# Kernel optimization log

Hardware: AMD Instinct MI355X
Metric: run time of the kernel (lower is better)

## Reference

```python
import jax, jax.numpy as jnp
import numpy as np

B, T, N, F, D, E = 8, 256, 118, 3, 128, 372
G = B * T  # number of graphs after flattening batch*time


def _gcn(x, src, dst, W, b):
    # x: [G, N, Fin] -> PyG GCNConv: X' = D^-1/2 (A+I) D^-1/2 (X W) + b
    h = x @ W  # [G, N, Fout]
    deg = jnp.ones((N,), h.dtype).at[dst].add(1.0)  # in-degree + self loop
    inv = deg ** -0.5
    norm = inv[src] * inv[dst]  # [E]
    agg = h * (1.0 / deg)[None, :, None]  # self-loop term: inv[i]*inv[i] = 1/deg
    agg = agg.at[:, dst].add(h[:, src] * norm[None, :, None])
    return agg + b


def _lstm_layer(x, Wih, Whh, bih, bhh):
    # x: [B, T, I]; PyTorch gate order i, f, g, o
    Bb, H = x.shape[0], Whh.shape[1]
    h0 = jnp.zeros((Bb, H), x.dtype)
    c0 = jnp.zeros((Bb, H), x.dtype)

    def step(carry, xt):
        h, c = carry
        gates = xt @ Wih.T + h @ Whh.T + bih + bhh
        i, f, g, o = jnp.split(gates, 4, axis=-1)
        c = jax.nn.sigmoid(f) * c + jax.nn.sigmoid(i) * jnp.tanh(g)
        h = jax.nn.sigmoid(o) * jnp.tanh(c)
        return (h, c), h

    _, ys = jax.lax.scan(step, (h0, c0), jnp.swapaxes(x, 0, 1))
    return jnp.swapaxes(ys, 0, 1)


def setup_inputs() -> dict:
    key = jax.random.key(0)
    ks = jax.random.split(key, 24)
    s = 0.05

    def rn(i, shape):
        return jax.random.normal(ks[i], shape, jnp.float32) * s

    return {
        "snapshot_sequence": jax.random.normal(ks[0], (B, T, N, F), jnp.float32),
        "edge_index": jax.random.randint(ks[1], (2, E), 0, N, dtype=jnp.int64),
        "scale": jnp.ones((F,), jnp.float32),
        "shift": jnp.zeros((F,), jnp.float32),
        "W1": rn(2, (F, D)), "b1": jnp.zeros((D,), jnp.float32),
        "W2": rn(3, (D, D)), "b2": jnp.zeros((D,), jnp.float32),
        "W3": rn(4, (D, D)), "b3": jnp.zeros((D,), jnp.float32),
        "Wih0": rn(5, (4 * D, D)), "Whh0": rn(6, (4 * D, D)),
        "bih0": jnp.zeros((4 * D,), jnp.float32), "bhh0": jnp.zeros((4 * D,), jnp.float32),
        "Wih1": rn(7, (4 * D, D)), "Whh1": rn(8, (4 * D, D)),
        "bih1": jnp.zeros((4 * D,), jnp.float32), "bhh1": jnp.zeros((4 * D,), jnp.float32),
        "hW1": rn(9, (D, 128)), "hb1": jnp.zeros((128,), jnp.float32),
        "hW2": rn(10, (128, 64)), "hb2": jnp.zeros((64,), jnp.float32),
        "hW3": rn(11, (64, 2)), "hb3": jnp.zeros((2,), jnp.float32),
    }


def reference(snapshot_sequence, edge_index, scale, shift,
              W1, b1, W2, b2, W3, b3,
              Wih0, Whh0, bih0, bhh0, Wih1, Whh1, bih1, bhh1,
              hW1, hb1, hW2, hb2, hW3, hb3):
    src, dst = edge_index[0], edge_index[1]
    x = snapshot_sequence * scale + shift              # FeatureNormalizer
    x = x.reshape(G, N, F)                             # flatten batch*time graphs
    x = jax.nn.silu(_gcn(x, src, dst, W1, b1))         # GCNConv 1 (dropout = eval identity)
    x = jax.nn.silu(_gcn(x, src, dst, W2, b2))         # GCNConv 2
    x = jax.nn.silu(_gcn(x, src, dst, W3, b3))         # GCNConv 3
    emb = x.mean(axis=1)                               # global_mean_pool -> [G, D]
    emb = emb.reshape(B, T, D)
    h = _lstm_layer(emb, Wih0, Whh0, bih0, bhh0)       # 2-layer LSTM (eval: no dropout)
    h = _lstm_layer(h, Wih1, Whh1, bih1, bhh1)
    final = h[:, -1, :]                                # [B, D]
    y = jax.nn.silu(final @ hW1 + hb1)
    y = jax.nn.silu(y @ hW2 + hb2)
    y = y @ hW3 + hb3
    return jax.nn.softplus(y) + 1e-6                   # [B, 2]
```

## Files before the change

kernel.cpp:

```cpp
#include <hip/hip_runtime.h>
#include <math.h>

#define NN 118
#define EE 372
#define GG 2048
#define DD 128
#define TT 256
#define BB 8
#define FD 512

#define XS 136

typedef short bf16x8 __attribute__((ext_vector_type(8)));
typedef float f32x4  __attribute__((ext_vector_type(4)));
typedef _Float16 f16x2 __attribute__((ext_vector_type(2)));

__device__ __forceinline__ float frcp_(float x) { return __builtin_amdgcn_rcpf(x); }
__device__ __forceinline__ float sig_f(float x) { return frcp_(1.0f + __expf(-x)); }
__device__ __forceinline__ float tanh_f(float x) { return 1.0f - 2.0f * frcp_(__expf(2.0f * x) + 1.0f); }
__device__ __forceinline__ float silu_f(float x) { return x * frcp_(1.0f + __expf(-x)); }
__device__ __forceinline__ float siluf_(float x) { return x / (1.0f + expf(-x)); }

__device__ __forceinline__ float fdot2_(unsigned int a, unsigned int b, float c) {
#if defined(__has_builtin) && __has_builtin(__builtin_amdgcn_fdot2)
    return __builtin_amdgcn_fdot2(__builtin_bit_cast(f16x2, a),
                                  __builtin_bit_cast(f16x2, b), c, false);
#else
    f16x2 x = __builtin_bit_cast(f16x2, a), y = __builtin_bit_cast(f16x2, b);
    return c + (float)x[0] * (float)y[0] + (float)x[1] * (float)y[1];
#endif
}

__device__ __forceinline__ void bar_lds() {
    asm volatile("s_waitcnt lgkmcnt(0)\n\ts_barrier" ::: "memory");
}

__device__ __forceinline__ unsigned short f2bf(float x) {
    unsigned int u = __float_as_uint(x);
    unsigned int r = (u + 0x7fffu + ((u >> 16) & 1u)) >> 16;
    return (unsigned short)r;
}
__device__ __forceinline__ float bf2f(unsigned short b) {
    return __uint_as_float(((unsigned int)b) << 16);
}

__global__ void prep_kernel(const int* __restrict__ ei,
                            const float* __restrict__ bih0, const float* __restrict__ bhh0,
                            const float* __restrict__ bih1, const float* __restrict__ bhh1,
                            float* __restrict__ bias0, float* __restrict__ bias1,
                            unsigned short* __restrict__ AbG) {
    __shared__ int sflag;
    __shared__ int ssrc[EE], sdst[EE];
    __shared__ int scount[NN];
    __shared__ float sinv[NN];
    __shared__ float Adense[NN * NN];
    int tid = threadIdx.x;
    if (tid == 0) sflag = 0;
    __syncthreads();
    for (int i = tid; i < 2 * EE; i += blockDim.x)
        if ((i & 1) && ei[i] != 0) atomicOr(&sflag, 1);
    __syncthreads();
    bool m64 = (sflag == 0);
    for (int e = tid; e < EE; e += blockDim.x) {
        int s, d;
        if (m64) { s = ei[2 * e]; d = ei[2 * EE + 2 * e]; }
        else     { s = ei[e];     d = ei[EE + e]; }
        s = min(max(s, 0), NN - 1); d = min(max(d, 0), NN - 1);
        ssrc[e] = s; sdst[e] = d;
    }
    for (int n = tid; n < NN; n += blockDim.x) scount[n] = 0;
    for (int i = tid; i < NN * NN; i += blockDim.x) Adense[i] = 0.0f;
    __syncthreads();
    for (int e = tid; e < EE; e += blockDim.x) atomicAdd(&scount[sdst[e]], 1);
    __syncthreads();
    for (int n = tid; n < NN; n += blockDim.x) {
        float deg = 1.0f + (float)scount[n];
        sinv[n] = rsqrtf(deg);
        Adense[n * NN + n] = 1.0f / deg;
    }
    __syncthreads();
    for (int e = tid; e < EE; e += blockDim.x)
        atomicAdd(&Adense[sdst[e] * NN + ssrc[e]], sinv[ssrc[e]] * sinv[sdst[e]]);
    __syncthreads();
    for (int i = tid; i < 128 * 128; i += blockDim.x) {
        int r = i >> 7, c = i & 127;
        AbG[i] = (r < NN && c < NN) ? f2bf(Adense[r * NN + c]) : (unsigned short)0;
    }
    for (int j = tid; j < FD; j += blockDim.x) {
        bias0[j] = bih0[j] + bhh0[j];
        bias1[j] = bih1[j] + bhh1[j];
    }
}

__global__ void convw_kernel(const float* __restrict__ W, unsigned short* __restrict__ out) {
    int i = blockIdx.x * 512 + threadIdx.x;
    int n = i >> 7, k = i & 127;
    out[i] = f2bf(W[k * DD + n]);
}

__global__ void convh_kernel(const float* __restrict__ W, unsigned int* __restrict__ out) {
    int i = blockIdx.x * 512 + threadIdx.x;
    int d = i & 127;
    int rest = i >> 7;
    int quarter = rest & 3;
    int qg = rest >> 2;
    int q = qg & 15, g = qg >> 4;
    const float* row = W + (size_t)(g * 128 + d) * 128 + quarter * 32;
    float a = row[2 * q], b = row[2 * q + 1];
    unsigned short lo = __builtin_bit_cast(unsigned short, (_Float16)a);
    unsigned short hi = __builtin_bit_cast(unsigned short, (_Float16)b);
    out[i] = (unsigned int)lo | ((unsigned int)hi << 16);
}

__global__ void transpose_kernel(const float* __restrict__ in, float* __restrict__ out) {
    int idx = blockIdx.x * blockDim.x + threadIdx.x;
    int j = idx >> 7, k = idx & 127;
    out[k * FD + j] = in[idx];
}

__device__ __forceinline__ void load_m(const unsigned short* __restrict__ src,
                                       unsigned short* __restrict__ dst, int tid) {
    const uint4* s4 = (const uint4*)src;
    for (int c = tid; c < 2048; c += 512) {
        int r = c >> 4, k8 = (c & 15) * 8;
        uint4 v = s4[c];
        *(uint4*)(dst + r * XS + k8) = v;
    }
}

__device__ __forceinline__ void mm_xw(const unsigned short* __restrict__ xb,
                                      const unsigned short* __restrict__ wt,
                                      unsigned short* __restrict__ hS, int tid) {
    int lane = tid & 63, w = tid >> 6;
    int lm = lane & 15, lq = lane >> 4;
    int wm = (w & 1) * 64, wn = (w >> 1) * 32;
    f32x4 acc[4][2];
#pragma unroll
    for (int mt = 0; mt < 4; ++mt)
#pragma unroll
        for (int nt = 0; nt < 2; ++nt) acc[mt][nt] = (f32x4){0.f, 0.f, 0.f, 0.f};
#pragma unroll
    for (int kb = 0; kb < 4; ++kb) {
        int ko = kb * 32 + lq * 8;
        bf16x8 b0 = *(const bf16x8*)(wt + (wn + lm) * XS + ko);
        bf16x8 b1 = *(const bf16x8*)(wt + (wn + 16 + lm) * XS + ko);
#pragma unroll
        for (int mt = 0; mt < 4; ++mt) {
            bf16x8 af = *(const bf16x8*)(xb + (wm + mt * 16 + lm) * XS + ko);
            acc[mt][0] = __builtin_amdgcn_mfma_f32_16x16x32_bf16(af, b0, acc[mt][0], 0, 0, 0);
            acc[mt][1] = __builtin_amdgcn_mfma_f32_16x16x32_bf16(af, b1, acc[mt][1], 0, 0, 0);
        }
    }
#pragma unroll
    for (int mt = 0; mt < 4; ++mt)
#pragma unroll
        for (int nt = 0; nt < 2; ++nt) {
            f32x4 a = acc[mt][nt];
            ushort4 pk;
            pk.x = f2bf(a[0]); pk.y = f2bf(a[1]); pk.z = f2bf(a[2]); pk.w = f2bf(a[3]);
            *(ushort4*)(hS + (wn + nt * 16 + lm) * XS + wm + mt * 16 + lq * 4) = pk;
        }
}

__device__ __forceinline__ void mm_agg(const unsigned short* __restrict__ Ab,
                                       const unsigned short* __restrict__ hS,
                                       unsigned short* __restrict__ xb,
                                       float bn0, float bn1, int tid) {
    int lane = tid & 63, w = tid >> 6;
    int lm = lane & 15, lq = lane >> 4;
    int wm = (w & 1) * 64, wn = (w >> 1) * 32;
    f32x4 acc[4][2];
#pragma unroll
    for (int mt = 0; mt < 4; ++mt)
#pragma unroll
        for (int nt = 0; nt < 2; ++nt) acc[mt][nt] = (f32x4){0.f, 0.f, 0.f, 0.f};
#pragma unroll
    for (int kb = 0; kb < 4; ++kb) {
        int ko = kb * 32 + lq * 8;
        bf16x8 b0 = *(const bf16x8*)(hS + (wn + lm) * XS + ko);
        bf16x8 b1 = *(const bf16x8*)(hS + (wn + 16 + lm) * XS + ko);
#pragma unroll
        for (int mt = 0; mt < 4; ++mt) {
            bf16x8 af = *(const bf16x8*)(Ab + (wm + mt * 16 + lm) * XS + ko);
            acc[mt][0] = __builtin_amdgcn_mfma_f32_16x16x32_bf16(af, b0, acc[mt][0], 0, 0, 0);
            acc[mt][1] = __builtin_amdgcn_mfma_f32_16x16x32_bf16(af, b1, acc[mt][1], 0, 0, 0);
        }
    }
#pragma unroll
    for (int mt = 0; mt < 4; ++mt)
#pragma unroll
        for (int nt = 0; nt < 2; ++nt) {
            float bn = nt ? bn1 : bn0;
            int col = wn + nt * 16 + lm;
#pragma unroll
            for (int i = 0; i < 4; ++i) {
                float v = silu_f(acc[mt][nt][i] + bn);
                xb[(wm + mt * 16 + lq * 4 + i) * XS + col] = f2bf(v);
            }
        }
}

__global__ __launch_bounds__(512) void gcn_kernel(
    const float* __restrict__ xg, const float* __restrict__ scale, const float* __restrict__ shift,
    const float* __restrict__ W1, const float* __restrict__ b1,
    const float* __restrict__ b2, const float* __restrict__ b3,
    const unsigned short* __restrict__ AbG,
    const unsigned short* __restrict__ Wt2g, const unsigned short* __restrict__ Wt3g,
    float* __restrict__ emb) {
    extern __shared__ char smem[];
    unsigned short* xb = (unsigned short*)smem;
    unsigned short* hS = (unsigned short*)(smem + 34816);
    unsigned short* Ab = (unsigned short*)(smem + 69632);
    unsigned short* wt = (unsigned short*)(smem + 104448);
    float* xinL  = (float*)(smem + 139264);
    float* meanS = (float*)(smem + 140688);
    int tid = threadIdx.x;
    int lane = tid & 63, w = tid >> 6;
    int g = blockIdx.x;

    for (int i = tid; i < 2176; i += 512) ((uint4*)hS)[i] = (uint4){0, 0, 0, 0};
    for (int i = tid; i < 170; i += 512) ((uint4*)(xb + NN * XS))[i] = (uint4){0, 0, 0, 0};
    float s0 = scale[0], s1 = scale[1], s2 = scale[2];
    float t0 = shift[0], t1 = shift[1], t2 = shift[2];
    const float* xrow = xg + (size_t)g * (NN * 3);
    for (int i = tid; i < NN * 3; i += 512) {
        int f = i % 3;
        float sc = (f == 0) ? s0 : ((f == 1) ? s1 : s2);
        float sf = (f == 0) ? t0 : ((f == 1) ? t1 : t2);
        xinL[i] = xrow[i] * sc + sf;
    }
    load_m(AbG, Ab, tid);
    load_m(Wt2g, wt, tid);
    int lm = lane & 15;
    int wn = (w >> 1) * 32;
    int n0 = wn + lm, n1 = wn + 16 + lm;
    float b1a = b1[n0], b1b = b1[n1];
    float b2a = b2[n0], b2b = b2[n1];
    float b3a = b3[n0], b3b = b3[n1];
    int dd = lane * 2;
    float2 w10 = *(const float2*)(W1 + dd);
    float2 w11 = *(const float2*)(W1 + DD + dd);
    float2 w12 = *(const float2*)(W1 + 2 * DD + dd);
    bar_lds();
    for (int k = 0; k < 15; ++k) {
        int n = w + 8 * k;
        if (n >= NN) break;
        float x0 = xinL[n * 3], x1 = xinL[n * 3 + 1], x2 = xinL[n * 3 + 2];
        hS[dd * XS + n]       = f2bf(x0 * w10.x + x1 * w11.x + x2 * w12.x);
        hS[(dd + 1) * XS + n] = f2bf(x0 * w10.y + x1 * w11.y + x2 * w12.y);
    }
    bar_lds();
    mm_agg(Ab, hS, xb, b1a, b1b, tid);
    bar_lds();
    mm_xw(xb, wt, hS, tid);
    bar_lds();
    load_m(Wt3g, wt, tid);
    mm_agg(Ab, hS, xb, b2a, b2b, tid);
    bar_lds();
    mm_xw(xb, wt, hS, tid);
    bar_lds();
    mm_agg(Ab, hS, xb, b3a, b3b, tid);
    bar_lds();
    {
        int d = tid & 127, part = tid >> 7;
        int a0 = part * 30;
        int a1 = (a0 + 30 < NN) ? (a0 + 30) : NN;
        float s = 0.f;
        for (int n = a0; n < a1; ++n) s += bf2f(xb[n * XS + d]);
        meanS[part * 128 + d] = s;
    }
    bar_lds();
    if (tid < 128) {
        float s = meanS[tid] + meanS[128 + tid] + meanS[256 + tid] + meanS[384 + tid];
        emb[(size_t)g * DD + tid] = s * (1.0f / (float)NN);
    }
}

__global__ __launch_bounds__(512) void proj_kernel(const float* __restrict__ src,
                                                   const float* __restrict__ WT,
                                                   const float* __restrict__ bias,
                                                   float* __restrict__ dst) {
    __shared__ __align__(16) float eL[DD];
    int g = blockIdx.x, tid = threadIdx.x;
    if (tid < DD) eL[tid] = src[(size_t)g * DD + tid];
    __syncthreads();
    float acc = bias[tid];
    const float* wt = WT + tid;
#pragma unroll 8
    for (int k = 0; k < DD; ++k) acc += eL[k] * wt[(size_t)k * FD];
    dst[(size_t)g * FD + tid] = acc;
}

__global__ __launch_bounds__(512, 2) void scan_kernel(
    const float* __restrict__ inp,
    const unsigned int* __restrict__ Wc,
    float* __restrict__ hout, int full) {
    __shared__ __align__(16) unsigned short hL[DD];
    __shared__ __align__(16) float sgP[3 * DD * 4];
    int b = blockIdx.x, j = threadIdx.x;
    int d = j & 127, quarter = j >> 7;
    unsigned int wreg[4][16];
#pragma unroll
    for (int g = 0; g < 4; ++g)
#pragma unroll
        for (int q = 0; q < 16; ++q)
            wreg[g][q] = Wc[(((g * 16 + q) << 2) + quarter) * 128 + d];
#pragma unroll
    for (int g = 0; g < 4; ++g)
#pragma unroll
        for (int q = 0; q < 16; ++q)
            asm volatile("" : "+v"(wreg[g][q]));
    if (j < 64) ((unsigned int*)hL)[j] = 0u;
    float creg = 0.f;
    const float* ib = inp + (size_t)b * TT * FD;
    float* hb_ = hout + (size_t)b * (full ? TT * DD : DD);
    float xg0[4], xg1[4];
    if (quarter == 0) {
#pragma unroll
        for (int g = 0; g < 4; ++g) { xg0[g] = ib[g * DD + d]; xg1[g] = ib[FD + g * DD + d]; }
    }
    bar_lds();
    for (int t = 0; t < TT; ++t) {
        float xg2[4];
        if (quarter == 0) {
            bool more = (t + 2 < TT);
#pragma unroll
            for (int g = 0; g < 4; ++g)
                xg2[g] = more ? ib[(t + 2) * FD + g * DD + d] : 0.f;
        }
        const uint4* h4 = (const uint4*)(hL + quarter * 32);
        float a0 = 0.f, a1 = 0.f, a2 = 0.f, a3 = 0.f;
#pragma unroll
        for (int c = 0; c < 4; ++c) {
            uint4 hv = h4[c];
            a0 = fdot2_(wreg[0][4 * c + 0], hv.x, a0);
            a1 = fdot2_(wreg[1][4 * c + 0], hv.x, a1);
            a2 = fdot2_(wreg[2][4 * c + 0], hv.x, a2);
            a3 = fdot2_(wreg[3][4 * c + 0], hv.x, a3);
            a0 = fdot2_(wreg[0][4 * c + 1], hv.y, a0);
            a1 = fdot2_(wreg[1][4 * c + 1], hv.y, a1);
            a2 = fdot2_(wreg[2][4 * c + 1], hv.y, a2);
            a3 = fdot2_(wreg[3][4 * c + 1], hv.y, a3);
            a0 = fdot2_(wreg[0][4 * c + 2], hv.z, a0);
            a1 = fdot2_(wreg[1][4 * c + 2], hv.z, a1);
            a2 = fdot2_(wreg[2][4 * c + 2], hv.z, a2);
            a3 = fdot2_(wreg[3][4 * c + 2], hv.z, a3);
            a0 = fdot2_(wreg[0][4 * c + 3], hv.w, a0);
            a1 = fdot2_(wreg[1][4 * c + 3], hv.w, a1);
            a2 = fdot2_(wreg[2][4 * c + 3], hv.w, a2);
            a3 = fdot2_(wreg[3][4 * c + 3], hv.w, a3);
        }
        if (quarter != 0)
            *(float4*)(sgP + ((quarter - 1) * DD + d) * 4) = make_float4(a0, a1, a2, a3);
        bar_lds();
        if (quarter == 0) {
            float4 p1 = *(const float4*)(sgP + d * 4);
            float4 p2 = *(const float4*)(sgP + (DD + d) * 4);
            float4 p3 = *(const float4*)(sgP + (2 * DD + d) * 4);
            float iv = sig_f(a0 + p1.x + p2.x + p3.x + xg0[0]);
            float fv = sig_f(a1 + p1.y + p2.y + p3.y + xg0[1]);
            float gv = tanh_f(a2 + p1.z + p2.z + p3.z + xg0[2]);
            float ov = sig_f(a3 + p1.w + p2.w + p3.w + xg0[3]);
            float cn = fv * creg + iv * gv;
            creg = cn;
            float hn = ov * tanh_f(cn);
            ((_Float16*)hL)[d] = (_Float16)hn;
            if (full) hb_[t * DD + d] = hn;
            else if (t == TT - 1) hb_[d] = hn;
#pragma unroll
            for (int g = 0; g < 4; ++g) { xg0[g] = xg1[g]; xg1[g] = xg2[g]; }
        }
        bar_lds();
    }
}

__global__ void head_kernel(const float* __restrict__ hfin,
                            const float* __restrict__ hW1, const float* __restrict__ hb1,
                            const float* __restrict__ hW2, const float* __restrict__ hb2,
                            const float* __restrict__ hW3, const float* __restrict__ hb3,
                            float* __restrict__ out) {
    __shared__ float fh[BB * DD];
    __shared__ float y1[BB * DD];
    __shared__ float y2[BB * 64];
    int tid = threadIdx.x;
    for (int i = tid; i < BB * DD; i += 256) fh[i] = hfin[i];
    __syncthreads();
    for (int i = tid; i < BB * DD; i += 256) {
        int bb = i >> 7, jj = i & 127;
        float acc = hb1[jj];
        for (int k = 0; k < DD; ++k) acc += fh[(bb << 7) + k] * hW1[(k << 7) + jj];
        y1[i] = siluf_(acc);
    }
    __syncthreads();
    for (int i = tid; i < BB * 64; i += 256) {
        int bb = i >> 6, jj = i & 63;
        float acc = hb2[jj];
        for (int k = 0; k < DD; ++k) acc += y1[(bb << 7) + k] * hW2[(k << 6) + jj];
        y2[i] = siluf_(acc);
    }
    __syncthreads();
    if (tid < BB * 2) {
        int bb = tid >> 1, m = tid & 1;
        float acc = hb3[m];
        for (int k = 0; k < 64; ++k) acc += y2[(bb << 6) + k] * hW3[k * 2 + m];
        float sp = fmaxf(acc, 0.f) + log1pf(expf(-fabsf(acc)));
        out[tid] = sp + 1e-6f;
    }
}

extern "C" void kernel_launch(void* const* d_in, const int* in_sizes, int n_in,
                              void* d_out, int out_size, void* d_ws, size_t ws_size,
                              hipStream_t stream) {
    const float* snap  = (const float*)d_in[0];
    const int*   edges = (const int*)d_in[1];
    const float* scale = (const float*)d_in[2];
    const float* shift = (const float*)d_in[3];
    const float* W1 = (const float*)d_in[4];
    const float* b1 = (const float*)d_in[5];
    const float* W2 = (const float*)d_in[6];
    const float* b2 = (const float*)d_in[7];
    const float* W3 = (const float*)d_in[8];
    const float* b3 = (const float*)d_in[9];
    const float* Wih0 = (const float*)d_in[10];
    const float* Whh0 = (const float*)d_in[11];
    const float* bih0 = (const float*)d_in[12];
    const float* bhh0 = (const float*)d_in[13];
    const float* Wih1 = (const float*)d_in[14];
    const float* Whh1 = (const float*)d_in[15];
    const float* bih1 = (const float*)d_in[16];
    const float* bhh1 = (const float*)d_in[17];
    const float* hW1 = (const float*)d_in[18];
    const float* hb1 = (const float*)d_in[19];
    const float* hW2 = (const float*)d_in[20];
    const float* hb2 = (const float*)d_in[21];
    const float* hW3 = (const float*)d_in[22];
    const float* hb3 = (const float*)d_in[23];

    float* ws = (float*)d_ws;
    float* bias0 = ws + 0;
    float* bias1 = ws + 512;
    unsigned short* AbG  = (unsigned short*)(ws + 1024);
    unsigned short* Wt2g = (unsigned short*)(ws + 9216);
    unsigned short* Wt3g = (unsigned short*)(ws + 17408);
    float* WT0 = ws + 25600;
    float* WT1 = ws + 91136;
    unsigned int* Wc0 = (unsigned int*)(ws + 156672);
    unsigned int* Wc1 = (unsigned int*)(ws + 189440);
    float* emb   = ws + 222208;
    float* inp   = ws + 484352;
    float* h0seq = ws + 1532928;
    float* hfin  = ws + 1795072;

    const int smem_gcn = 142736;
    hipFuncSetAttribute((const void*)gcn_kernel,
                        hipFuncAttributeMaxDynamicSharedMemorySize, smem_gcn);

    prep_kernel<<<1, 256, 0, stream>>>(edges, bih0, bhh0, bih1, bhh1,
                                       bias0, bias1, AbG);
    convw_kernel<<<32, 512, 0, stream>>>(W2, Wt2g);
    convw_kernel<<<32, 512, 0, stream>>>(W3, Wt3g);
    convh_kernel<<<64, 512, 0, stream>>>(Whh0, Wc0);
    convh_kernel<<<64, 512, 0, stream>>>(Whh1, Wc1);
    transpose_kernel<<<128, 512, 0, stream>>>(Wih0, WT0);
    transpose_kernel<<<128, 512, 0, stream>>>(Wih1, WT1);
    gcn_kernel<<<GG, 512, smem_gcn, stream>>>(snap, scale, shift, W1, b1, b2, b3,
                                              AbG, Wt2g, Wt3g, emb);
    proj_kernel<<<GG, 512, 0, stream>>>(emb, WT0, bias0, inp);
    scan_kernel<<<BB, 512, 0, stream>>>(inp, Wc0, h0seq, 1);
    proj_kernel<<<GG, 512, 0, stream>>>(h0seq, WT1, bias1, inp);
    scan_kernel<<<BB, 512, 0, stream>>>(inp, Wc1, hfin, 0);
    head_kernel<<<1, 256, 0, stream>>>(hfin, hW1, hb1, hW2, hb2, hW3, hb3, (float*)d_out);
}
```

Measured before the change: 582.3 us.

## Give each thread one full gate row in LSTM scan, combine gates via DPP

The LSTM recurrence kernel now maps each thread to one gate row (d, g) holding the full 128-wide fp16 weight row in registers, instead of splitting the K dimension into quarters that had to be reduced through shared memory. The four gates of a hidden unit sit in adjacent lanes and are exchanged with DPP quad permutes. One unified sigmoid/tanh formula is evaluated per lane, and the h vector is double-buffered so each step needs one barrier instead of two. The weight-packing kernel is changed to the matching layout. This removes the partial-sum LDS round trip and a barrier per timestep, but needs 64 weight registers per thread and drops occupancy to one block per CU.

```diff
diff --git a/kernel.cpp b/kernel.cpp
--- a/kernel.cpp
+++ b/kernel.cpp
@@ -100,16 +100,13 @@
 
 __global__ void convh_kernel(const float* __restrict__ W, unsigned int* __restrict__ out) {
     int i = blockIdx.x * 512 + threadIdx.x;
-    int d = i & 127;
-    int rest = i >> 7;
-    int quarter = rest & 3;
-    int qg = rest >> 2;
-    int q = qg & 15, g = qg >> 4;
-    const float* row = W + (size_t)(g * 128 + d) * 128 + quarter * 32;
-    float a = row[2 * q], b = row[2 * q + 1];
+    int jj = i >> 6, q = i & 63;
+    int d = jj >> 2, g = jj & 3;
+    const float* row = W + (size_t)(g * 128 + d) * 128 + 2 * q;
+    float a = row[0], b = row[1];
     unsigned short lo = __builtin_bit_cast(unsigned short, (_Float16)a);
     unsigned short hi = __builtin_bit_cast(unsigned short, (_Float16)b);
-    out[i] = (unsigned int)lo | ((unsigned int)hi << 16);
+    out[q * 512 + jj] = (unsigned int)lo | ((unsigned int)hi << 16);
 }
 
 __global__ void transpose_kernel(const float* __restrict__ in, float* __restrict__ out) {
@@ -291,85 +288,61 @@
     dst[(size_t)g * FD + tid] = acc;
 }
 
-__global__ __launch_bounds__(512, 2) void scan_kernel(
+__global__ __launch_bounds__(512, 1) void scan_kernel(
     const float* __restrict__ inp,
     const unsigned int* __restrict__ Wc,
     float* __restrict__ hout, int full) {
-    __shared__ __align__(16) unsigned short hL[DD];
-    __shared__ __align__(16) float sgP[3 * DD * 4];
+    __shared__ __align__(16) unsigned short hB[2][DD];
     int b = blockIdx.x, j = threadIdx.x;
-    int d = j & 127, quarter = j >> 7;
-    unsigned int wreg[4][16];
-#pragma unroll
-    for (int g = 0; g < 4; ++g)
-#pragma unroll
-        for (int q = 0; q < 16; ++q)
-            wreg[g][q] = Wc[(((g * 16 + q) << 2) + quarter) * 128 + d];
-#pragma unroll
-    for (int g = 0; g < 4; ++g)
-#pragma unroll
-        for (int q = 0; q < 16; ++q)
-            asm volatile("" : "+v"(wreg[g][q]));
-    if (j < 64) ((unsigned int*)hL)[j] = 0u;
-    float creg = 0.f;
+    int d = j >> 2, g = j & 3;
+    unsigned int wreg[64];
+#pragma unroll
+    for (int q = 0; q < 64; ++q) wreg[q] = Wc[q * 512 + j];
+#pragma unroll
+    for (int q = 0; q < 64; ++q) asm volatile("" : "+v"(wreg[q]));
+    if (j < 128) ((unsigned int*)hB)[j] = 0u;
     const float* ib = inp + (size_t)b * TT * FD;
     float* hb_ = hout + (size_t)b * (full ? TT * DD : DD);
-    float xg0[4], xg1[4];
-    if (quarter == 0) {
-#pragma unroll
-        for (int g = 0; g < 4; ++g) { xg0[g] = ib[g * DD + d]; xg1[g] = ib[FD + g * DD + d]; }
-    }
+    int poff = g * DD + d;
+    float m1  = (g == 2) ? 2.0f : 1.0f;
+    float nm1 = -m1;
+    float c1  = 1.0f - m1;
+    float creg = 0.f;
+    float xg0 = ib[poff], xg1 = ib[FD + poff];
+    int p = 0;
     bar_lds();
     for (int t = 0; t < TT; ++t) {
-        float xg2[4];
-        if (quarter == 0) {
-            bool more = (t + 2 < TT);
-#pragma unroll
-            for (int g = 0; g < 4; ++g)
-                xg2[g] = more ? ib[(t + 2) * FD + g * DD + d] : 0.f;
-        }
-        const uint4* h4 = (const uint4*)(hL + quarter * 32);
+        float xg2 = (t + 2 < TT) ? ib[(size_t)(t + 2) * FD + poff] : 0.f;
+        const uint4* h4 = (const uint4*)(hB[p]);
         float a0 = 0.f, a1 = 0.f, a2 = 0.f, a3 = 0.f;
 #pragma unroll
-        for (int c = 0; c < 4; ++c) {
+        for (int c = 0; c < 16; ++c) {
             uint4 hv = h4[c];
-            a0 = fdot2_(wreg[0][4 * c + 0], hv.x, a0);
-            a1 = fdot2_(wreg[1][4 * c + 0], hv.x, a1);
-            a2 = fdot2_(wreg[2][4 * c + 0], hv.x, a2);
-            a3 = fdot2_(wreg[3][4 * c + 0], hv.x, a3);
-            a0 = fdot2_(wreg[0][4 * c + 1], hv.y, a0);
-            a1 = fdot2_(wreg[1][4 * c + 1], hv.y, a1);
-            a2 = fdot2_(wreg[2][4 * c + 1], hv.y, a2);
-            a3 = fdot2_(wreg[3][4 * c + 1], hv.y, a3);
-            a0 = fdot2_(wreg[0][4 * c + 2], hv.z, a0);
-            a1 = fdot2_(wreg[1][4 * c + 2], hv.z, a1);
-            a2 = fdot2_(wreg[2][4 * c + 2], hv.z, a2);
-            a3 = fdot2_(wreg[3][4 * c + 2], hv.z, a3);
-            a0 = fdot2_(wreg[0][4 * c + 3], hv.w, a0);
-            a1 = fdot2_(wreg[1][4 * c + 3], hv.w, a1);
-            a2 = fdot2_(wreg[2][4 * c + 3], hv.w, a2);
-            a3 = fdot2_(wreg[3][4 * c + 3], hv.w, a3);
-        }
-        if (quarter != 0)
-            *(float4*)(sgP + ((quarter - 1) * DD + d) * 4) = make_float4(a0, a1, a2, a3);
-        bar_lds();
-        if (quarter == 0) {
-            float4 p1 = *(const float4*)(sgP + d * 4);
-            float4 p2 = *(const float4*)(sgP + (DD + d) * 4);
-            float4 p3 = *(const float4*)(sgP + (2 * DD + d) * 4);
-            float iv = sig_f(a0 + p1.x + p2.x + p3.x + xg0[0]);
-            float fv = sig_f(a1 + p1.y + p2.y + p3.y + xg0[1]);
-            float gv = tanh_f(a2 + p1.z + p2.z + p3.z + xg0[2]);
-            float ov = sig_f(a3 + p1.w + p2.w + p3.w + xg0[3]);
-            float cn = fv * creg + iv * gv;
-            creg = cn;
-            float hn = ov * tanh_f(cn);
-            ((_Float16*)hL)[d] = (_Float16)hn;
-            if (full) hb_[t * DD + d] = hn;
-            else if (t == TT - 1) hb_[d] = hn;
-#pragma unroll
-            for (int g = 0; g < 4; ++g) { xg0[g] = xg1[g]; xg1[g] = xg2[g]; }
-        }
+            a0 = fdot2_(wreg[4 * c + 0], hv.x, a0);
+            a1 = fdot2_(wreg[4 * c + 1], hv.y, a1);
+            a2 = fdot2_(wreg[4 * c + 2], hv.z, a2);
+            a3 = fdot2_(wreg[4 * c + 3], hv.w, a3);
+        }
+        float pre = ((a0 + a1) + (a2 + a3)) + xg0;
+        float act = frcp_(1.0f + __expf(pre * nm1)) * m1 + c1;
+        int ai = __float_as_int(act);
+        float iv = __int_as_float(__builtin_amdgcn_update_dpp(0, ai, 0x00, 0xF, 0xF, true));
+        float fv = __int_as_float(__builtin_amdgcn_update_dpp(0, ai, 0x55, 0xF, 0xF, true));
+        float gv = __int_as_float(__builtin_amdgcn_update_dpp(0, ai, 0xAA, 0xF, 0xF, true));
+        float ov = __int_as_float(__builtin_amdgcn_update_dpp(0, ai, 0xFF, 0xF, 0xF, true));
+        float cn = fv * creg + iv * gv;
+        creg = cn;
+        float hn = ov * tanh_f(cn);
+        if (g == 0) {
+            ((_Float16*)hB[p ^ 1])[d] = (_Float16)hn;
+            if (full) {
+                hb_[t * DD + d] = hn;
+            } else if (t == TT - 1) {
+                hb_[d] = hn;
+            }
+        }
+        xg0 = xg1; xg1 = xg2;
+        p ^= 1;
         bar_lds();
     }
 }
```

After: 569.4 us. 2.2% less time.
